# Kernel tuning notes

Measured on AMD Instinct MI355X. Metric: run time of the kernel, lower is better.

The kernel has to match this reference:

```python
import jax, jax.numpy as jnp
import numpy as np

VOCAB = 30000  # opts.numofingr
EPS = 1e-12


def setup_inputs() -> dict:
    key = jax.random.key(0)
    ks = jax.random.split(key, 8)
    B, L = 4096, 20
    ingrs = jax.random.randint(ks[0], (B, L), 0, VOCAB, dtype=jnp.int32)
    lengths = jax.random.randint(ks[1], (B,), 0, 21, dtype=jnp.int32)
    # MLP params: Linear(VOCAB,512) -> ReLU -> Linear(512,1024) -> ReLU -> Linear(1024,2047)
    # Stored so that one-hot @ W1 == W1[ingr]; i.e. W1 has shape [VOCAB, 512].
    W1 = jax.random.normal(ks[2], (VOCAB, 512), dtype=jnp.float32) * (1.0 / np.sqrt(VOCAB))
    b1 = jax.random.normal(ks[3], (512,), dtype=jnp.float32) * 0.01
    W2 = jax.random.normal(ks[4], (512, 1024), dtype=jnp.float32) * (1.0 / np.sqrt(512))
    b2 = jax.random.normal(ks[5], (1024,), dtype=jnp.float32) * 0.01
    W3 = jax.random.normal(ks[6], (1024, 2047), dtype=jnp.float32) * (1.0 / np.sqrt(1024))
    b3 = jax.random.normal(ks[7], (2047,), dtype=jnp.float32) * 0.01
    return {"ingrs": ingrs, "lengths": lengths,
            "W1": W1, "b1": b1, "W2": W2, "b2": b2, "W3": W3, "b3": b3}


def reference(ingrs, lengths, W1, b1, W2, b2, W3, b3):
    # One-hot x MLP first layer == embedding row gather: [B, L, 512]
    h1 = jax.nn.relu(W1[ingrs] + b1)
    h2 = jax.nn.relu(jnp.einsum('blh,hk->blk', h1, W2) + b2)   # [B, L, 1024]
    emb = jnp.einsum('blk,ko->blo', h2, W3) + b3               # [B, L, 2047]
    # L2-normalize each ingredient embedding (torch norm(p=2, dim=1) on [1,2047])
    nrm = jnp.sqrt(jnp.sum(emb * emb, axis=-1, keepdims=True))
    emb = emb / jnp.maximum(nrm, EPS)
    # Masked sum over valid ingredients (ingr_ln truncation in the source)
    L = ingrs.shape[1]
    mask = (jnp.arange(L)[None, :] < lengths[:, None]).astype(emb.dtype)  # [B, L]
    return jnp.einsum('blo,bl->bo', emb, mask)                 # [B, 2047]
```

## Files before the change

### kernel.cpp

```cpp
#include <hip/hip_runtime.h>

#define VOCAB 30000
#define MPAD  30080
#define MT_PAD 240

typedef __attribute__((ext_vector_type(8))) short bf16x8;
typedef __attribute__((ext_vector_type(4))) float f32x4;

__device__ __forceinline__ unsigned short f2bf(float f) {
    unsigned int u = __builtin_bit_cast(unsigned int, f);
    u += 0x7fffu + ((u >> 16) & 1u);
    return (unsigned short)(u >> 16);
}
__device__ __forceinline__ float bf2f(unsigned int h) {
    unsigned int u = h << 16;
    return __builtin_bit_cast(float, u);
}

__device__ __forceinline__ void async16(const void* g, void* l) {
    __builtin_amdgcn_global_load_lds(
        (__attribute__((address_space(1))) void*)g,
        (__attribute__((address_space(3))) void*)l, 16, 0, 0);
}

__global__ void comp_mark(const int* __restrict__ ingrs, const int* __restrict__ lengths,
                          int* __restrict__ flags, int* __restrict__ cnt)
{
    const int i = blockIdx.x * 256 + threadIdx.x;
    if (i == 0) *cnt = 0;
    if (i >= 4096 * 20) return;
    const int b = i / 20;
    const int l = i - b * 20;
    if (l < lengths[b]) flags[ingrs[i]] = 1;
}

__global__ void comp_assign(const int* __restrict__ flags, int* __restrict__ remap,
                            int* __restrict__ cnt)
{
    const int i = blockIdx.x * 256 + threadIdx.x;
    if (i < VOCAB && flags[i] == 1) remap[i] = atomicAdd(cnt, 1);
}


__device__ __forceinline__ void transpose_body(
    const float* __restrict__ in, unsigned short* __restrict__ out,
    int K, int Nin, int n0, int k0, int tid, float (*t)[65])
{
#pragma unroll
    for (int p = 0; p < 16; ++p) {
        const int lin = p * 256 + tid;
        const int kk = lin >> 6, nn = lin & 63;
        const int n = n0 + nn;
        t[kk][nn] = (n < Nin) ? in[(size_t)(k0 + kk) * Nin + n] : 0.f;
    }
    __syncthreads();
#pragma unroll
    for (int p = 0; p < 16; ++p) {
        const int lin = p * 256 + tid;
        const int nn = lin >> 6, kk = lin & 63;
        out[(size_t)(n0 + nn) * K + k0 + kk] = f2bf(t[kk][nn]);
    }
}

__global__ __launch_bounds__(256)
void mega_prep(const float* __restrict__ W1, const float* __restrict__ b1,
               const int* __restrict__ flags, const int* __restrict__ remap,
               unsigned short* __restrict__ A1,
               const float* __restrict__ W2, unsigned short* __restrict__ W2T,
               const float* __restrict__ W3, unsigned short* __restrict__ W3T,
               const int* __restrict__ ingrs, const int* __restrict__ lengths,
               int* __restrict__ slots)
{
    __shared__ float t[64][65];
    const int bid = blockIdx.x;
    const int tid = threadIdx.x;

    if (bid < 15000) {
        const int id = bid * 2 + (tid >> 7);
        if (flags[id] != 1) return;
        const int row = remap[id];
        const int k4  = (tid & 127) * 4;
        const float4 w  = *(const float4*)(W1 + (size_t)id * 512 + k4);
        const float4 bb = *(const float4*)(b1 + k4);
        unsigned short o[4];
        o[0] = f2bf(fmaxf(w.x + bb.x, 0.f));
        o[1] = f2bf(fmaxf(w.y + bb.y, 0.f));
        o[2] = f2bf(fmaxf(w.z + bb.z, 0.f));
        o[3] = f2bf(fmaxf(w.w + bb.w, 0.f));
        *(uint2*)(A1 + (size_t)row * 512 + k4) = *(const uint2*)o;
    } else if (bid < 15128) {
        const int local = bid - 15000;
        transpose_body(W2, W2T, 512, 1024, (local & 15) * 64, (local >> 4) * 64, tid, t);
    } else if (bid < 15640) {
        const int local = bid - 15128;
        transpose_body(W3, W3T, 1024, 2047, (local & 31) * 64, (local >> 5) * 64, tid, t);
    } else {
        const int i = (bid - 15640) * 256 + tid;
        if (i >= 4096 * 20) return;
        const int b = i / 20;
        const int l = i - b * 20;
        if (l < lengths[b]) slots[i] = remap[ingrs[i]];
    }
}

__global__ __launch_bounds__(256)
void gemm_bf16(const unsigned short* __restrict__ A,
               const unsigned short* __restrict__ BT,
               const float* __restrict__ bias, int bias_n,
               unsigned short* __restrict__ C,
               int K, int N, int relu, const int* __restrict__ cnt, int nt_shift)
{
    const int id = blockIdx.x;
    const int w  = id >> 3;
    const int n_tile = w & ((1 << nt_shift) - 1);
    const int m_tile = (id & 7) + ((w >> nt_shift) << 3);
    const int m0 = m_tile * 128;
    const int mc = (*cnt + 127) & ~127;
    if (m0 >= mc) return;
    const int n0 = n_tile * 128;

    __shared__ __align__(16) unsigned short smem[128 * 136];
    unsigned short* As = smem;
    unsigned short* Bs = smem + 8192;

    const int tid  = threadIdx.x;
    const int lane = tid & 63;
    const int wid  = tid >> 6;
    const int wr   = wid >> 1;
    const int wc   = wid & 1;

    const int q  = lane >> 4;
    const int ml = lane & 15;

    f32x4 acc[4][4];
    const f32x4 zero = {0.f, 0.f, 0.f, 0.f};
#pragma unroll
    for (int i = 0; i < 4; ++i)
#pragma unroll
        for (int j = 0; j < 4; ++j) acc[i][j] = zero;

    const int rg = lane >> 3;
    const int kc = (lane & 7) ^ rg;
    const unsigned short* pA = A  + (size_t)(m0 + wid * 32 + rg) * K + kc * 8;
    const unsigned short* pB = BT + (size_t)(n0 + wid * 32 + rg) * K + kc * 8;
    unsigned short* lA = &As[wid * 4 * 512 + lane * 8];
    unsigned short* lB = &Bs[wid * 4 * 512 + lane * 8];

    const int swz0 = (q ^ (ml & 7)) * 8;

    for (int k0 = 0; k0 < K; k0 += 64) {
#pragma unroll
        for (int gg = 0; gg < 4; ++gg) {
            async16(pA + (size_t)gg * 8 * K, lA + gg * 512);
            async16(pB + (size_t)gg * 8 * K, lB + gg * 512);
        }
        pA += 64; pB += 64;
        __syncthreads();

        bf16x8 af[4], bfr[4];
#pragma unroll
        for (int t = 0; t < 4; ++t) {
            af[t]  = *(const bf16x8*)&As[(wr * 64 + t * 16 + ml) * 64 + swz0];
            bfr[t] = *(const bf16x8*)&Bs[(wc * 64 + t * 16 + ml) * 64 + swz0];
        }
#pragma unroll
        for (int i = 0; i < 4; ++i)
#pragma unroll
            for (int j = 0; j < 4; ++j)
                acc[i][j] = __builtin_amdgcn_mfma_f32_16x16x32_bf16(
                    af[i], bfr[j], acc[i][j], 0, 0, 0);
#pragma unroll
        for (int t = 0; t < 4; ++t) {
            af[t]  = *(const bf16x8*)&As[(wr * 64 + t * 16 + ml) * 64 + (swz0 ^ 32)];
            bfr[t] = *(const bf16x8*)&Bs[(wc * 64 + t * 16 + ml) * 64 + (swz0 ^ 32)];
        }
#pragma unroll
        for (int i = 0; i < 4; ++i)
#pragma unroll
            for (int j = 0; j < 4; ++j)
                acc[i][j] = __builtin_amdgcn_mfma_f32_16x16x32_bf16(
                    af[i], bfr[j], acc[i][j], 0, 0, 0);

        __syncthreads();
    }

#pragma unroll
    for (int i = 0; i < 4; ++i) {
#pragma unroll
        for (int j = 0; j < 4; ++j) {
#pragma unroll
            for (int r = 0; r < 4; ++r) {
                const int rl = wr * 64 + i * 16 + q * 4 + r;
                const int cl = wc * 64 + j * 16 + ml;
                float v = acc[i][j][r];
                const int col = n0 + cl;
                v += (col < bias_n) ? bias[col] : 0.f;
                if (relu) v = fmaxf(v, 0.f);
                smem[rl * 136 + cl] = f2bf(v);
            }
        }
    }
    __syncthreads();
#pragma unroll
    for (int p = 0; p < 8; ++p) {
        const int rr = p * 16 + (tid >> 4);
        const int cc = tid & 15;
        const uint4 val = *(const uint4*)&smem[rr * 136 + cc * 8];
        *(uint4*)&C[(size_t)(m0 + rr) * N + n0 + cc * 8] = val;
    }
}

__global__ __launch_bounds__(256)
void gather_norm_sum(const int* __restrict__ lengths, const int* __restrict__ slots,
                     const unsigned short* __restrict__ Table, float* __restrict__ out)
{
    const int b    = blockIdx.x;
    const int tid  = threadIdx.x;
    const int lane = tid & 63;
    const int wid  = tid >> 6;
    __shared__ float red[4];

    float acc[8];
#pragma unroll
    for (int j = 0; j < 8; ++j) acc[j] = 0.f;

    const int len = lengths[b];
    if (len > 0) {
        int slot = slots[b * 20];
        uint4 u = *((const uint4*)(Table + (size_t)slot * 2048) + tid);
        for (int l = 0; l < len; ++l) {
            const uint4 cu = u;
            if (l + 1 < len) {
                const int ns = slots[b * 20 + l + 1];
                u = *((const uint4*)(Table + (size_t)ns * 2048) + tid);
            }
            float v[8];
            v[0] = bf2f(cu.x & 0xffffu); v[1] = bf2f(cu.x >> 16);
            v[2] = bf2f(cu.y & 0xffffu); v[3] = bf2f(cu.y >> 16);
            v[4] = bf2f(cu.z & 0xffffu); v[5] = bf2f(cu.z >> 16);
            v[6] = bf2f(cu.w & 0xffffu); v[7] = bf2f(cu.w >> 16);
            float s = 0.f;
#pragma unroll
            for (int j = 0; j < 8; ++j) s += v[j] * v[j];
#pragma unroll
            for (int off = 1; off < 64; off <<= 1) s += __shfl_xor(s, off, 64);
            if (lane == 0) red[wid] = s;
            __syncthreads();
            const float tot  = red[0] + red[1] + red[2] + red[3];
            const float invn = 1.0f / fmaxf(sqrtf(tot), 1e-12f);
            __syncthreads();
#pragma unroll
            for (int j = 0; j < 8; ++j) acc[j] += v[j] * invn;
        }
    }

    const size_t base = (size_t)b * 2047;
#pragma unroll
    for (int j = 0; j < 8; ++j) {
        const int col = tid * 8 + j;
        if (col < 2047) out[base + col] = acc[j];
    }
}


extern "C" void kernel_launch(void* const* d_in, const int* in_sizes, int n_in,
                              void* d_out, int out_size, void* d_ws, size_t ws_size,
                              hipStream_t stream)
{
    const int*   ingrs   = (const int*)d_in[0];
    const int*   lengths = (const int*)d_in[1];
    const float* W1 = (const float*)d_in[2];
    const float* b1 = (const float*)d_in[3];
    const float* W2 = (const float*)d_in[4];
    const float* b2 = (const float*)d_in[5];
    const float* W3 = (const float*)d_in[6];
    const float* b3 = (const float*)d_in[7];
    float* out = (float*)d_out;

    char* ws = (char*)d_ws;
    unsigned short* A1    = (unsigned short*)(ws);
    unsigned short* H2    = (unsigned short*)(ws + 30801920);
    unsigned short* Table = (unsigned short*)(ws + 92405760);
    unsigned short* W2T   = (unsigned short*)(ws + 215613440);
    unsigned short* W3T   = (unsigned short*)(ws + 216662016);
    int*            flags = (int*)(ws + 220856320);
    int*            remap = (int*)(ws + 220976320);
    int*            cnt   = (int*)(ws + 221096320);
    int*            slots = (int*)(ws + 221216448);

    comp_mark  <<<(4096 * 20 + 255) / 256, 256, 0, stream>>>(ingrs, lengths, flags, cnt);
    comp_assign<<<(VOCAB + 255) / 256, 256, 0, stream>>>(flags, remap, cnt);
    mega_prep<<<15960, 256, 0, stream>>>(W1, b1, flags, remap, A1,
                                         W2, W2T, W3, W3T, ingrs, lengths, slots);

    gemm_bf16<<<MT_PAD * 8, 256, 0, stream>>>(
        A1, W2T, b2, 1024, H2, 512, 1024, 1, cnt, 3);
    gemm_bf16<<<MT_PAD * 16, 256, 0, stream>>>(
        H2, W3T, b3, 2047, Table, 1024, 2048, 0, cnt, 4);

    gather_norm_sum<<<4096, 256, 0, stream>>>(lengths, slots, Table, out);
}
```

Baseline: 342.1 us.

## Move W3 transpose and slot fill into first GEMM launch; single-wave gather

Moves the W3 transpose and the slot-index fill out of the prep kernel and into extra blocks of the first GEMM launch, so that work can run alongside GEMM1 instead of ahead of it. The gather/normalize kernel now uses one 64-lane wavefront per batch row, with each lane handling 32 elements, so the norm reduction needs no shared memory or __syncthreads. In exchange, the gather kernel holds more registers per lane and launches fewer threads, and GEMM1 blocks share the launch with transpose blocks.

```diff
diff --git a/kernel.cpp b/kernel.cpp
--- a/kernel.cpp
+++ b/kernel.cpp
@@ -23,8 +23,8 @@
         (__attribute__((address_space(3))) void*)l, 16, 0, 0);
 }
 
-__global__ void comp_mark(const int* __restrict__ ingrs, const int* __restrict__ lengths,
-                          int* __restrict__ flags, int* __restrict__ cnt)
+__global__ void k_mark(const int* __restrict__ ingrs, const int* __restrict__ lengths,
+                       int* __restrict__ flags, int* __restrict__ cnt)
 {
     const int i = blockIdx.x * 256 + threadIdx.x;
     if (i == 0) *cnt = 0;
@@ -34,8 +34,8 @@
     if (l < lengths[b]) flags[ingrs[i]] = 1;
 }
 
-__global__ void comp_assign(const int* __restrict__ flags, int* __restrict__ remap,
-                            int* __restrict__ cnt)
+__global__ void k_assign(const int* __restrict__ flags, int* __restrict__ remap,
+                         int* __restrict__ cnt)
 {
     const int i = blockIdx.x * 256 + threadIdx.x;
     if (i < VOCAB && flags[i] == 1) remap[i] = atomicAdd(cnt, 1);
@@ -62,14 +62,113 @@
     }
 }
 
+__device__ __forceinline__ void gemm_body(
+    unsigned short* smem,
+    const unsigned short* __restrict__ A, const unsigned short* __restrict__ BT,
+    const float* __restrict__ bias, int bias_n, unsigned short* __restrict__ C,
+    int K, int N, int relu, int mc, int id, int nt_shift)
+{
+    const int w  = id >> 3;
+    const int n_tile = w & ((1 << nt_shift) - 1);
+    const int m_tile = (id & 7) + ((w >> nt_shift) << 3);
+    const int m0 = m_tile * 128;
+    if (m0 >= mc) return;
+    const int n0 = n_tile * 128;
+
+    unsigned short* As = smem;
+    unsigned short* Bs = smem + 8192;
+
+    const int tid  = threadIdx.x;
+    const int lane = tid & 63;
+    const int wid  = tid >> 6;
+    const int wr   = wid >> 1;
+    const int wc   = wid & 1;
+    const int q  = lane >> 4;
+    const int ml = lane & 15;
+
+    f32x4 acc[4][4];
+    const f32x4 zero = {0.f, 0.f, 0.f, 0.f};
+#pragma unroll
+    for (int i = 0; i < 4; ++i)
+#pragma unroll
+        for (int j = 0; j < 4; ++j) acc[i][j] = zero;
+
+    const int rg = lane >> 3;
+    const int kc = (lane & 7) ^ rg;
+    const unsigned short* pA = A  + (size_t)(m0 + wid * 32 + rg) * K + kc * 8;
+    const unsigned short* pB = BT + (size_t)(n0 + wid * 32 + rg) * K + kc * 8;
+    unsigned short* lA = &As[wid * 4 * 512 + lane * 8];
+    unsigned short* lB = &Bs[wid * 4 * 512 + lane * 8];
+
+    const int swz0 = (q ^ (ml & 7)) * 8;
+
+    for (int k0 = 0; k0 < K; k0 += 64) {
+#pragma unroll
+        for (int gg = 0; gg < 4; ++gg) {
+            async16(pA + (size_t)gg * 8 * K, lA + gg * 512);
+            async16(pB + (size_t)gg * 8 * K, lB + gg * 512);
+        }
+        pA += 64; pB += 64;
+        __syncthreads();
+
+        bf16x8 af[4], bfr[4];
+#pragma unroll
+        for (int t = 0; t < 4; ++t) {
+            af[t]  = *(const bf16x8*)&As[(wr * 64 + t * 16 + ml) * 64 + swz0];
+            bfr[t] = *(const bf16x8*)&Bs[(wc * 64 + t * 16 + ml) * 64 + swz0];
+        }
+#pragma unroll
+        for (int i = 0; i < 4; ++i)
+#pragma unroll
+            for (int j = 0; j < 4; ++j)
+                acc[i][j] = __builtin_amdgcn_mfma_f32_16x16x32_bf16(
+                    af[i], bfr[j], acc[i][j], 0, 0, 0);
+#pragma unroll
+        for (int t = 0; t < 4; ++t) {
+            af[t]  = *(const bf16x8*)&As[(wr * 64 + t * 16 + ml) * 64 + (swz0 ^ 32)];
+            bfr[t] = *(const bf16x8*)&Bs[(wc * 64 + t * 16 + ml) * 64 + (swz0 ^ 32)];
+        }
+#pragma unroll
+        for (int i = 0; i < 4; ++i)
+#pragma unroll
+            for (int j = 0; j < 4; ++j)
+                acc[i][j] = __builtin_amdgcn_mfma_f32_16x16x32_bf16(
+                    af[i], bfr[j], acc[i][j], 0, 0, 0);
+
+        __syncthreads();
+    }
+
+#pragma unroll
+    for (int i = 0; i < 4; ++i) {
+#pragma unroll
+        for (int j = 0; j < 4; ++j) {
+#pragma unroll
+            for (int r = 0; r < 4; ++r) {
+                const int rl = wr * 64 + i * 16 + q * 4 + r;
+                const int cl = wc * 64 + j * 16 + ml;
+                float v = acc[i][j][r];
+                const int col = n0 + cl;
+                v += (col < bias_n) ? bias[col] : 0.f;
+                if (relu) v = fmaxf(v, 0.f);
+                smem[rl * 136 + cl] = f2bf(v);
+            }
+        }
+    }
+    __syncthreads();
+#pragma unroll
+    for (int p = 0; p < 8; ++p) {
+        const int rr = p * 16 + (tid >> 4);
+        const int cc = tid & 15;
+        const uint4 val = *(const uint4*)&smem[rr * 136 + cc * 8];
+        *(uint4*)&C[(size_t)(m0 + rr) * N + n0 + cc * 8] = val;
+    }
+}
+
 __global__ __launch_bounds__(256)
-void mega_prep(const float* __restrict__ W1, const float* __restrict__ b1,
-               const int* __restrict__ flags, const int* __restrict__ remap,
-               unsigned short* __restrict__ A1,
-               const float* __restrict__ W2, unsigned short* __restrict__ W2T,
-               const float* __restrict__ W3, unsigned short* __restrict__ W3T,
-               const int* __restrict__ ingrs, const int* __restrict__ lengths,
-               int* __restrict__ slots)
+void k_prep(const float* __restrict__ W1, const float* __restrict__ b1,
+            const int* __restrict__ flags, const int* __restrict__ remap,
+            unsigned short* __restrict__ A1,
+            const float* __restrict__ W2, unsigned short* __restrict__ W2T)
 {
     __shared__ float t[64][65];
     const int bid = blockIdx.x;
@@ -88,177 +187,105 @@
         o[2] = f2bf(fmaxf(w.z + bb.z, 0.f));
         o[3] = f2bf(fmaxf(w.w + bb.w, 0.f));
         *(uint2*)(A1 + (size_t)row * 512 + k4) = *(const uint2*)o;
-    } else if (bid < 15128) {
+    } else {
         const int local = bid - 15000;
         transpose_body(W2, W2T, 512, 1024, (local & 15) * 64, (local >> 4) * 64, tid, t);
-    } else if (bid < 15640) {
-        const int local = bid - 15128;
-        transpose_body(W3, W3T, 1024, 2047, (local & 31) * 64, (local >> 5) * 64, tid, t);
+    }
+}
+
+__global__ __launch_bounds__(256)
+void k_gemm1(const unsigned short* __restrict__ A1, const unsigned short* __restrict__ W2T,
+             const float* __restrict__ b2, unsigned short* __restrict__ H2,
+             const int* __restrict__ cnt,
+             const float* __restrict__ W3, unsigned short* __restrict__ W3T,
+             const int* __restrict__ ingrs, const int* __restrict__ lengths,
+             const int* __restrict__ remap, int* __restrict__ slots)
+{
+    __shared__ __align__(16) unsigned short smem[128 * 136];
+    const int bid = blockIdx.x;
+    if (bid < MT_PAD * 8) {
+        const int mc = (*cnt + 127) & ~127;
+        gemm_body(smem, A1, W2T, b2, 1024, H2, 512, 1024, 1, mc, bid, 3);
+    } else if (bid < MT_PAD * 8 + 512) {
+        const int local = bid - MT_PAD * 8;
+        transpose_body(W3, W3T, 1024, 2047, (local & 31) * 64, (local >> 5) * 64,
+                       threadIdx.x, (float(*)[65])smem);
     } else {
-        const int i = (bid - 15640) * 256 + tid;
-        if (i >= 4096 * 20) return;
-        const int b = i / 20;
-        const int l = i - b * 20;
-        if (l < lengths[b]) slots[i] = remap[ingrs[i]];
+        const int i = (bid - (MT_PAD * 8 + 512)) * 256 + threadIdx.x;
+        if (i < 4096 * 20) {
+            const int b = i / 20;
+            const int l = i - b * 20;
+            if (l < lengths[b]) slots[i] = remap[ingrs[i]];
+        }
     }
 }
 
 __global__ __launch_bounds__(256)
-void gemm_bf16(const unsigned short* __restrict__ A,
-               const unsigned short* __restrict__ BT,
-               const float* __restrict__ bias, int bias_n,
-               unsigned short* __restrict__ C,
-               int K, int N, int relu, const int* __restrict__ cnt, int nt_shift)
-{
-    const int id = blockIdx.x;
-    const int w  = id >> 3;
-    const int n_tile = w & ((1 << nt_shift) - 1);
-    const int m_tile = (id & 7) + ((w >> nt_shift) << 3);
-    const int m0 = m_tile * 128;
+void k_gemm2(const unsigned short* __restrict__ H2, const unsigned short* __restrict__ W3T,
+             const float* __restrict__ b3, unsigned short* __restrict__ Table,
+             const int* __restrict__ cnt)
+{
+    __shared__ __align__(16) unsigned short smem[128 * 136];
     const int mc = (*cnt + 127) & ~127;
-    if (m0 >= mc) return;
-    const int n0 = n_tile * 128;
-
-    __shared__ __align__(16) unsigned short smem[128 * 136];
-    unsigned short* As = smem;
-    unsigned short* Bs = smem + 8192;
-
-    const int tid  = threadIdx.x;
-    const int lane = tid & 63;
-    const int wid  = tid >> 6;
-    const int wr   = wid >> 1;
-    const int wc   = wid & 1;
-
-    const int q  = lane >> 4;
-    const int ml = lane & 15;
-
-    f32x4 acc[4][4];
-    const f32x4 zero = {0.f, 0.f, 0.f, 0.f};
-#pragma unroll
-    for (int i = 0; i < 4; ++i)
-#pragma unroll
-        for (int j = 0; j < 4; ++j) acc[i][j] = zero;
-
-    const int rg = lane >> 3;
-    const int kc = (lane & 7) ^ rg;
-    const unsigned short* pA = A  + (size_t)(m0 + wid * 32 + rg) * K + kc * 8;
-    const unsigned short* pB = BT + (size_t)(n0 + wid * 32 + rg) * K + kc * 8;
-    unsigned short* lA = &As[wid * 4 * 512 + lane * 8];
-    unsigned short* lB = &Bs[wid * 4 * 512 + lane * 8];
-
-    const int swz0 = (q ^ (ml & 7)) * 8;
-
-    for (int k0 = 0; k0 < K; k0 += 64) {
-#pragma unroll
-        for (int gg = 0; gg < 4; ++gg) {
-            async16(pA + (size_t)gg * 8 * K, lA + gg * 512);
-            async16(pB + (size_t)gg * 8 * K, lB + gg * 512);
-        }
-        pA += 64; pB += 64;
-        __syncthreads();
-
-        bf16x8 af[4], bfr[4];
-#pragma unroll
-        for (int t = 0; t < 4; ++t) {
-            af[t]  = *(const bf16x8*)&As[(wr * 64 + t * 16 + ml) * 64 + swz0];
-            bfr[t] = *(const bf16x8*)&Bs[(wc * 64 + t * 16 + ml) * 64 + swz0];
-        }
-#pragma unroll
-        for (int i = 0; i < 4; ++i)
-#pragma unroll
-            for (int j = 0; j < 4; ++j)
-                acc[i][j] = __builtin_amdgcn_mfma_f32_16x16x32_bf16(
-                    af[i], bfr[j], acc[i][j], 0, 0, 0);
-#pragma unroll
-        for (int t = 0; t < 4; ++t) {
-            af[t]  = *(const bf16x8*)&As[(wr * 64 + t * 16 + ml) * 64 + (swz0 ^ 32)];
-            bfr[t] = *(const bf16x8*)&Bs[(wc * 64 + t * 16 + ml) * 64 + (swz0 ^ 32)];
-        }
-#pragma unroll
-        for (int i = 0; i < 4; ++i)
-#pragma unroll
-            for (int j = 0; j < 4; ++j)
-                acc[i][j] = __builtin_amdgcn_mfma_f32_16x16x32_bf16(
-                    af[i], bfr[j], acc[i][j], 0, 0, 0);
-
-        __syncthreads();
-    }
-
-#pragma unroll
-    for (int i = 0; i < 4; ++i) {
-#pragma unroll
-        for (int j = 0; j < 4; ++j) {
-#pragma unroll
-            for (int r = 0; r < 4; ++r) {
-                const int rl = wr * 64 + i * 16 + q * 4 + r;
-                const int cl = wc * 64 + j * 16 + ml;
-                float v = acc[i][j][r];
-                const int col = n0 + cl;
-                v += (col < bias_n) ? bias[col] : 0.f;
-                if (relu) v = fmaxf(v, 0.f);
-                smem[rl * 136 + cl] = f2bf(v);
-            }
-        }
-    }
-    __syncthreads();
-#pragma unroll
-    for (int p = 0; p < 8; ++p) {
-        const int rr = p * 16 + (tid >> 4);
-        const int cc = tid & 15;
-        const uint4 val = *(const uint4*)&smem[rr * 136 + cc * 8];
-        *(uint4*)&C[(size_t)(m0 + rr) * N + n0 + cc * 8] = val;
-    }
-}
-
-__global__ __launch_bounds__(256)
-void gather_norm_sum(const int* __restrict__ lengths, const int* __restrict__ slots,
-                     const unsigned short* __restrict__ Table, float* __restrict__ out)
+    gemm_body(smem, H2, W3T, b3, 2047, Table, 1024, 2048, 0, mc, blockIdx.x, 4);
+}
+
+__global__ __launch_bounds__(64)
+void k_gather(const int* __restrict__ lengths, const int* __restrict__ slots,
+              const unsigned short* __restrict__ Table, float* __restrict__ out)
 {
     const int b    = blockIdx.x;
-    const int tid  = threadIdx.x;
-    const int lane = tid & 63;
-    const int wid  = tid >> 6;
-    __shared__ float red[4];
-
-    float acc[8];
-#pragma unroll
-    for (int j = 0; j < 8; ++j) acc[j] = 0.f;
+    const int lane = threadIdx.x;
+
+    float acc[32];
+#pragma unroll
+    for (int j = 0; j < 32; ++j) acc[j] = 0.f;
 
     const int len = lengths[b];
     if (len > 0) {
-        int slot = slots[b * 20];
-        uint4 u = *((const uint4*)(Table + (size_t)slot * 2048) + tid);
+        uint4 u[4];
+        {
+            const int slot = slots[b * 20];
+            const uint4* rp = (const uint4*)(Table + (size_t)slot * 2048);
+#pragma unroll
+            for (int c = 0; c < 4; ++c) u[c] = rp[c * 64 + lane];
+        }
         for (int l = 0; l < len; ++l) {
-            const uint4 cu = u;
+            uint4 cu[4];
+#pragma unroll
+            for (int c = 0; c < 4; ++c) cu[c] = u[c];
             if (l + 1 < len) {
                 const int ns = slots[b * 20 + l + 1];
-                u = *((const uint4*)(Table + (size_t)ns * 2048) + tid);
+                const uint4* rp = (const uint4*)(Table + (size_t)ns * 2048);
+#pragma unroll
+                for (int c = 0; c < 4; ++c) u[c] = rp[c * 64 + lane];
             }
-            float v[8];
-            v[0] = bf2f(cu.x & 0xffffu); v[1] = bf2f(cu.x >> 16);
-            v[2] = bf2f(cu.y & 0xffffu); v[3] = bf2f(cu.y >> 16);
-            v[4] = bf2f(cu.z & 0xffffu); v[5] = bf2f(cu.z >> 16);
-            v[6] = bf2f(cu.w & 0xffffu); v[7] = bf2f(cu.w >> 16);
+            float v[32];
+#pragma unroll
+            for (int c = 0; c < 4; ++c) {
+                v[c*8+0] = bf2f(cu[c].x & 0xffffu); v[c*8+1] = bf2f(cu[c].x >> 16);
+                v[c*8+2] = bf2f(cu[c].y & 0xffffu); v[c*8+3] = bf2f(cu[c].y >> 16);
+                v[c*8+4] = bf2f(cu[c].z & 0xffffu); v[c*8+5] = bf2f(cu[c].z >> 16);
+                v[c*8+6] = bf2f(cu[c].w & 0xffffu); v[c*8+7] = bf2f(cu[c].w >> 16);
+            }
             float s = 0.f;
 #pragma unroll
-            for (int j = 0; j < 8; ++j) s += v[j] * v[j];
+            for (int j = 0; j < 32; ++j) s += v[j] * v[j];
 #pragma unroll
             for (int off = 1; off < 64; off <<= 1) s += __shfl_xor(s, off, 64);
-            if (lane == 0) red[wid] = s;
-            __syncthreads();
-            const float tot  = red[0] + red[1] + red[2] + red[3];
-            const float invn = 1.0f / fmaxf(sqrtf(tot), 1e-12f);
-            __syncthreads();
-#pragma unroll
-            for (int j = 0; j < 8; ++j) acc[j] += v[j] * invn;
+            const float invn = 1.0f / fmaxf(sqrtf(s), 1e-12f);
+#pragma unroll
+            for (int j = 0; j < 32; ++j) acc[j] += v[j] * invn;
         }
     }
 
     const size_t base = (size_t)b * 2047;
 #pragma unroll
-    for (int j = 0; j < 8; ++j) {
-        const int col = tid * 8 + j;
-        if (col < 2047) out[base + col] = acc[j];
+    for (int c = 0; c < 4; ++c) {
+        const int col = (c * 64 + lane) * 8;
+#pragma unroll
+        for (int j = 0; j < 8; ++j)
+            if (col + j < 2047) out[base + col + j] = acc[c * 8 + j];
     }
 }
 
@@ -288,15 +315,12 @@
     int*            cnt   = (int*)(ws + 221096320);
     int*            slots = (int*)(ws + 221216448);
 
-    comp_mark  <<<(4096 * 20 + 255) / 256, 256, 0, stream>>>(ingrs, lengths, flags, cnt);
-    comp_assign<<<(VOCAB + 255) / 256, 256, 0, stream>>>(flags, remap, cnt);
-    mega_prep<<<15960, 256, 0, stream>>>(W1, b1, flags, remap, A1,
-                                         W2, W2T, W3, W3T, ingrs, lengths, slots);
-
-    gemm_bf16<<<MT_PAD * 8, 256, 0, stream>>>(
-        A1, W2T, b2, 1024, H2, 512, 1024, 1, cnt, 3);
-    gemm_bf16<<<MT_PAD * 16, 256, 0, stream>>>(
-        H2, W3T, b3, 2047, Table, 1024, 2048, 0, cnt, 4);
-
-    gather_norm_sum<<<4096, 256, 0, stream>>>(lengths, slots, Table, out);
-}
+    k_mark  <<<(4096 * 20 + 255) / 256, 256, 0, stream>>>(ingrs, lengths, flags, cnt);
+    k_assign<<<(VOCAB + 255) / 256, 256, 0, stream>>>(flags, remap, cnt);
+    k_prep<<<15128, 256, 0, stream>>>(W1, b1, flags, remap, A1, W2, W2T);
+    k_gemm1<<<MT_PAD * 8 + 512 + 320, 256, 0, stream>>>(
+        A1, W2T, b2, H2, cnt, W3, W3T, ingrs, lengths, remap, slots);
+    k_gemm2<<<MT_PAD * 16, 256, 0, stream>>>(H2, W3T, b3, Table, cnt);
+
+    k_gather<<<4096, 64, 0, stream>>>(lengths, slots, Table, out);
+}
```

Result: faster. 328.5 us (-4.0%).
